# Optimization experiments

Measured on AMD Instinct MI355X. Metric: run time of the kernel, lower is better.

Reference implementation:

```python
import jax, jax.numpy as jnp
import numpy as np

BATCH, FIELD_DIM, EMBED_DIM = 4096, 20000, 64


def setup_inputs() -> dict:
    key = jax.random.key(0)
    k_idx, k_w = jax.random.split(key)
    # multi-hot indicator matrix (values in {0,1})
    indices = jax.random.randint(k_idx, (BATCH, FIELD_DIM), 0, 2, dtype=jnp.int32)
    # kaiming_normal_ on (field_dim, embed_dim): std = sqrt(2 / fan_in), fan_in = embed_dim
    W = jax.random.normal(k_w, (FIELD_DIM, EMBED_DIM), dtype=jnp.float32) * np.sqrt(2.0 / EMBED_DIM)
    return {"indices": indices, "W": W}


def reference(indices, W):
    # Per row: gather embeddings at nonzero positions and sum ('sum' aggregate).
    # Equivalent to binary-mask @ W; rows with no nonzeros yield zeros naturally.
    mask = (indices != 0).astype(W.dtype)          # [B, F]
    out = jnp.einsum('bf,fd->bd', mask, W)         # [B, D]
    return out
```

## Files before the change

kernel.cpp:

```cpp
#include <hip/hip_runtime.h>
#include <hip/hip_bf16.h>

#define BATCH 4096
#define FIELD 20000
#define EMBED 64
#define KSTEPS 625
#define KC     25
#define SPW    25
#define MTILES 256
#define TOTAL_WAVES (MTILES * KC)

typedef __attribute__((ext_vector_type(4))) float  f32x4;
typedef __attribute__((ext_vector_type(8))) short  short8;
typedef __attribute__((ext_vector_type(4))) int    i32x4;
typedef __attribute__((ext_vector_type(4))) unsigned int u32x4;

__global__ __launch_bounds__(256) void zero_out_kernel(float* __restrict__ out) {
    out[blockIdx.x * 256 + threadIdx.x] = 0.0f;
}

__device__ __forceinline__ unsigned bf16_rtne(float f) {
    unsigned u = __builtin_bit_cast(unsigned, f);
    return (u + 0x7FFFu + ((u >> 16) & 1u)) >> 16;
}

__global__ __launch_bounds__(256) void prep_w_kernel(const float* __restrict__ W,
                                                     unsigned int* __restrict__ Wswz) {
    int o2 = blockIdx.x * 256 + threadIdx.x;
    if (o2 >= FIELD * EMBED / 2) return;
    int j    = (o2 & 3) * 2;
    int lane = (o2 >> 2) & 63;
    int t    = (o2 >> 8) & 3;
    int s    =  o2 >> 10;
    int k    = 32 * s + ((lane >> 4) << 3) + j;
    int col  = 16 * t + (lane & 15);
    float w0 = W[(size_t)k * EMBED + col];
    float w1 = W[(size_t)(k + 1) * EMBED + col];
    Wswz[o2] = bf16_rtne(w0) | (bf16_rtne(w1) << 16);
}

__global__ __launch_bounds__(256) void emb_mfma_kernel(const int* __restrict__ idxm,
                                                       const unsigned int* __restrict__ Wswz,
                                                       float* __restrict__ out) {
    const int lane  = threadIdx.x & 63;
    const int w     = blockIdx.x * 4 + (threadIdx.x >> 6);
    const int mtile = w % MTILES;
    const int kc    = w / MTILES;
    const int lrow  = lane & 15;
    const int khi   = lane >> 4;
    const int row   = mtile * 16 + lrow;

    const i32x4* pA = (const i32x4*)(idxm + (size_t)row * FIELD
                                     + (size_t)kc * SPW * 32 + khi * 8);
    const short8* pB = (const short8*)Wswz + (size_t)kc * SPW * 4 * 64 + lane;

    f32x4 acc0 = {0.f, 0.f, 0.f, 0.f};
    f32x4 acc1 = acc0, acc2 = acc0, acc3 = acc0;

#pragma unroll 5
    for (int s = 0; s < SPW; ++s) {
        i32x4 x = pA[0];
        i32x4 y = pA[1];
        pA += 8;

        unsigned m0 = (x.x != 0 ? 0x3F80u : 0u) | (x.y != 0 ? 0x3F800000u : 0u);
        unsigned m1 = (x.z != 0 ? 0x3F80u : 0u) | (x.w != 0 ? 0x3F800000u : 0u);
        unsigned m2 = (y.x != 0 ? 0x3F80u : 0u) | (y.y != 0 ? 0x3F800000u : 0u);
        unsigned m3 = (y.z != 0 ? 0x3F80u : 0u) | (y.w != 0 ? 0x3F800000u : 0u);
        u32x4 av = {m0, m1, m2, m3};
        short8 afrag = __builtin_bit_cast(short8, av);

        short8 b0 = pB[0];
        short8 b1 = pB[64];
        short8 b2 = pB[128];
        short8 b3 = pB[192];
        pB += 256;

        acc0 = __builtin_amdgcn_mfma_f32_16x16x32_bf16(afrag, b0, acc0, 0, 0, 0);
        acc1 = __builtin_amdgcn_mfma_f32_16x16x32_bf16(afrag, b1, acc1, 0, 0, 0);
        acc2 = __builtin_amdgcn_mfma_f32_16x16x32_bf16(afrag, b2, acc2, 0, 0, 0);
        acc3 = __builtin_amdgcn_mfma_f32_16x16x32_bf16(afrag, b3, acc3, 0, 0, 0);
    }

    float* obase = out + (size_t)mtile * 16 * EMBED;
#pragma unroll
    for (int i = 0; i < 4; ++i) {
        int orow = khi * 4 + i;
        atomicAdd(obase + (size_t)orow * EMBED +      lrow, acc0[i]);
        atomicAdd(obase + (size_t)orow * EMBED + 16 + lrow, acc1[i]);
        atomicAdd(obase + (size_t)orow * EMBED + 32 + lrow, acc2[i]);
        atomicAdd(obase + (size_t)orow * EMBED + 48 + lrow, acc3[i]);
    }
}

extern "C" void kernel_launch(void* const* d_in, const int* in_sizes, int n_in,
                              void* d_out, int out_size, void* d_ws, size_t ws_size,
                              hipStream_t stream) {
    const int*   idxm = (const int*)d_in[0];
    const float* W    = (const float*)d_in[1];
    float*       out  = (float*)d_out;
    unsigned int* Wswz = (unsigned int*)d_ws;

    hipLaunchKernelGGL(zero_out_kernel, dim3(BATCH * EMBED / 256), dim3(256), 0, stream, out);
    hipLaunchKernelGGL(prep_w_kernel, dim3(FIELD * EMBED / 2 / 256), dim3(256), 0, stream, W, Wswz);
    hipLaunchKernelGGL(emb_mfma_kernel, dim3(TOTAL_WAVES / 4), dim3(256), 0, stream,
                       idxm, Wswz, out);
}
```

Before: 104.7 us.

## Replace atomic split-K accumulation with partial buffer and reduce kernel; LDS-transpose W prep

Each split-K wave now writes its partial 16x64 tile to a workspace buffer instead of issuing float atomics into the output. A separate reduce kernel sums the 25 partials, which removes the zero-out kernel and the atomic contention. The W prep kernel now loads coalesced float4 rows into LDS and writes swizzled bf16 fragments as 16-byte stores, replacing strided global reads. The cost is an extra kernel launch and about 26 MB of partial-sum traffic, and it relies on the workspace being large enough to hold the partials.

```diff
diff --git a/kernel.cpp b/kernel.cpp
--- a/kernel.cpp
+++ b/kernel.cpp
@@ -9,15 +9,13 @@
 #define SPW    25
 #define MTILES 256
 #define TOTAL_WAVES (MTILES * KC)
+#define WSWZ_DWORDS (FIELD * EMBED / 2)
+#define PART_STRIDE (MTILES * 1024)
 
 typedef __attribute__((ext_vector_type(4))) float  f32x4;
 typedef __attribute__((ext_vector_type(8))) short  short8;
 typedef __attribute__((ext_vector_type(4))) int    i32x4;
 typedef __attribute__((ext_vector_type(4))) unsigned int u32x4;
-
-__global__ __launch_bounds__(256) void zero_out_kernel(float* __restrict__ out) {
-    out[blockIdx.x * 256 + threadIdx.x] = 0.0f;
-}
 
 __device__ __forceinline__ unsigned bf16_rtne(float f) {
     unsigned u = __builtin_bit_cast(unsigned, f);
@@ -26,22 +24,37 @@
 
 __global__ __launch_bounds__(256) void prep_w_kernel(const float* __restrict__ W,
                                                      unsigned int* __restrict__ Wswz) {
-    int o2 = blockIdx.x * 256 + threadIdx.x;
-    if (o2 >= FIELD * EMBED / 2) return;
-    int j    = (o2 & 3) * 2;
-    int lane = (o2 >> 2) & 63;
-    int t    = (o2 >> 8) & 3;
-    int s    =  o2 >> 10;
-    int k    = 32 * s + ((lane >> 4) << 3) + j;
-    int col  = 16 * t + (lane & 15);
-    float w0 = W[(size_t)k * EMBED + col];
-    float w1 = W[(size_t)(k + 1) * EMBED + col];
-    Wswz[o2] = bf16_rtne(w0) | (bf16_rtne(w1) << 16);
+    __shared__ float lds[32 * 65];
+    const int t  = threadIdx.x;
+    const int s0 = blockIdx.x;
+
+    const float4* src = (const float4*)(W + (size_t)s0 * 2048);
+    float4 a = src[t * 2 + 0];
+    float4 b = src[t * 2 + 1];
+    int l  = t * 8;
+    int kl = l >> 6, c = l & 63;
+    float* dst = lds + kl * 65 + c;
+    dst[0] = a.x; dst[1] = a.y; dst[2] = a.z; dst[3] = a.w;
+    dst[4] = b.x; dst[5] = b.y; dst[6] = b.z; dst[7] = b.w;
+    __syncthreads();
+
+    const int lane = t & 63, tq = t >> 6;
+    const int khi = lane >> 4, lrow = lane & 15;
+    const int col = tq * 16 + lrow;
+    u32x4 o;
+#pragma unroll
+    for (int j2 = 0; j2 < 4; ++j2) {
+        int kloc = khi * 8 + 2 * j2;
+        float w0 = lds[kloc * 65 + col];
+        float w1 = lds[(kloc + 1) * 65 + col];
+        o[j2] = bf16_rtne(w0) | (bf16_rtne(w1) << 16);
+    }
+    *(u32x4*)(Wswz + ((size_t)(s0 * 4 + tq) * 64 + lane) * 4) = o;
 }
 
 __global__ __launch_bounds__(256) void emb_mfma_kernel(const int* __restrict__ idxm,
                                                        const unsigned int* __restrict__ Wswz,
-                                                       float* __restrict__ out) {
+                                                       float* __restrict__ P) {
     const int lane  = threadIdx.x & 63;
     const int w     = blockIdx.x * 4 + (threadIdx.x >> 6);
     const int mtile = w % MTILES;
@@ -82,15 +95,28 @@
         acc3 = __builtin_amdgcn_mfma_f32_16x16x32_bf16(afrag, b3, acc3, 0, 0, 0);
     }
 
-    float* obase = out + (size_t)mtile * 16 * EMBED;
+    float* pP = P + (size_t)(kc * MTILES + mtile) * 1024 + lane * 4;
+    *(f32x4*)(pP + 0)   = acc0;
+    *(f32x4*)(pP + 256) = acc1;
+    *(f32x4*)(pP + 512) = acc2;
+    *(f32x4*)(pP + 768) = acc3;
+}
+
+__global__ __launch_bounds__(256) void reduce_kernel(const float* __restrict__ P,
+                                                     float* __restrict__ out) {
+    const int tid = blockIdx.x * 256 + threadIdx.x;
+    float s = 0.f;
 #pragma unroll
-    for (int i = 0; i < 4; ++i) {
-        int orow = khi * 4 + i;
-        atomicAdd(obase + (size_t)orow * EMBED +      lrow, acc0[i]);
-        atomicAdd(obase + (size_t)orow * EMBED + 16 + lrow, acc1[i]);
-        atomicAdd(obase + (size_t)orow * EMBED + 32 + lrow, acc2[i]);
-        atomicAdd(obase + (size_t)orow * EMBED + 48 + lrow, acc3[i]);
-    }
+    for (int kc = 0; kc < KC; ++kc)
+        s += P[(size_t)kc * PART_STRIDE + tid];
+
+    const int i     = tid & 3;
+    const int lane  = (tid >> 2) & 63;
+    const int f     = (tid >> 8) & 3;
+    const int mtile = tid >> 10;
+    const int row   = mtile * 16 + (lane >> 4) * 4 + i;
+    const int col   = f * 16 + (lane & 15);
+    out[(size_t)row * EMBED + col] = s;
 }
 
 extern "C" void kernel_launch(void* const* d_in, const int* in_sizes, int n_in,
@@ -99,10 +125,13 @@
     const int*   idxm = (const int*)d_in[0];
     const float* W    = (const float*)d_in[1];
     float*       out  = (float*)d_out;
+
     unsigned int* Wswz = (unsigned int*)d_ws;
+    float*        P    = (float*)((char*)d_ws + (size_t)WSWZ_DWORDS * 4);
 
-    hipLaunchKernelGGL(zero_out_kernel, dim3(BATCH * EMBED / 256), dim3(256), 0, stream, out);
-    hipLaunchKernelGGL(prep_w_kernel, dim3(FIELD * EMBED / 2 / 256), dim3(256), 0, stream, W, Wswz);
+    hipLaunchKernelGGL(prep_w_kernel, dim3(KSTEPS), dim3(256), 0, stream, W, Wswz);
     hipLaunchKernelGGL(emb_mfma_kernel, dim3(TOTAL_WAVES / 4), dim3(256), 0, stream,
-                       idxm, Wswz, out);
+                       idxm, Wswz, P);
+    hipLaunchKernelGGL(reduce_kernel, dim3(BATCH * EMBED / 256), dim3(256), 0, stream,
+                       P, out);
 }
```

New measurement: 106.1 us. Within noise of the previous version (+1.3%).
